# Kernel tuning notes

Measured on AMD Instinct MI355X. Metric: run time of the kernel, lower is better.

Reference implementation:

```python
import jax, jax.numpy as jnp
import numpy as np

EPS = 1e-5
OFFSET_SCALE = 1.0
KPTS = 9   # 3x3 deformable kernel
GROUP = 1  # in_dim // out_dim


def _bn(x, g, b, m, v):
    # eval-mode BatchNorm2d on (B,C,H,W)
    s = g / jnp.sqrt(v + EPS)
    return x * s[None, :, None, None] + (b - m * s)[None, :, None, None]


def _dcnv4_core(value, offset, mask, offset_scale):
    # value: (B,H,W,G,Cg); offset: (B,H,W,G,K,2) as (dx,dy); mask: (B,H,W,G,K)
    B, H, W, G, Cg = value.shape
    K = mask.shape[-1]
    dt = value.dtype
    ky = jnp.repeat(jnp.arange(3) - 1, 3).astype(dt)
    kx = jnp.tile(jnp.arange(3) - 1, 3).astype(dt)
    grid = jnp.stack([kx, ky], -1)                                   # (K,2)
    base = jnp.stack(jnp.meshgrid(jnp.arange(W, dtype=dt),
                                  jnp.arange(H, dtype=dt),
                                  indexing='xy'), -1)                # (H,W,2) = (x,y)
    loc = base[None, :, :, None, None, :] + (grid + offset) * offset_scale  # (B,H,W,G,K,2)
    px, py = loc[..., 0], loc[..., 1]
    x0 = jnp.floor(px); y0 = jnp.floor(py)
    fx = px - x0; fy = py - y0
    vflat = value.transpose(0, 3, 1, 2, 4).reshape(B, G, H * W, Cg)
    out = jnp.zeros((B, G, H * W, Cg), dt)
    corners = ((0.0, 0.0, (1 - fx) * (1 - fy)), (1.0, 0.0, fx * (1 - fy)),
               (0.0, 1.0, (1 - fx) * fy), (1.0, 1.0, fx * fy))
    for dx, dy, wgt in corners:
        xi = x0 + dx; yi = y0 + dy
        valid = ((xi >= 0) & (xi < W) & (yi >= 0) & (yi < H)).astype(dt)
        idx = (jnp.clip(yi, 0, W and H - 1) * W + jnp.clip(xi, 0, W - 1)).astype(jnp.int32)
        idx = idx.transpose(0, 3, 1, 2, 4).reshape(B, G, H * W * K)
        v = jnp.take_along_axis(vflat, idx[..., None], axis=2).reshape(B, G, H * W, K, Cg)
        w = (wgt * valid * mask).transpose(0, 3, 1, 2, 4).reshape(B, G, H * W, K)
        out = out + jnp.einsum('bgsk,bgskc->bgsc', w, v)
    return out.reshape(B, G, H, W, Cg).transpose(0, 2, 3, 1, 4).reshape(B, H, W, G * Cg)


def setup_inputs() -> dict:
    key = jax.random.key(0)
    B, C, H, W = 8, 128, 64, 64
    C_OUT = 128
    OM = ((GROUP * KPTS * 3 + 7) // 8) * 8  # 32, offset_mask padded width
    ks = jax.random.split(key, 16)
    f = jnp.float32
    sc = 1.0 / np.sqrt(C).astype(np.float32)
    return {
        'x': jax.random.normal(ks[0], (B, C, H, W), f),
        'bn1_g': jax.random.uniform(ks[1], (C,), f, 0.5, 1.5),
        'bn1_b': jax.random.normal(ks[2], (C,), f) * 0.1,
        'bn1_m': jax.random.normal(ks[3], (C,), f) * 0.1,
        'bn1_v': jax.random.uniform(ks[4], (C,), f, 0.5, 1.5),
        'w_pw0': jax.random.normal(ks[5], (C, C), f) * sc,
        'w_vp': jax.random.normal(ks[6], (C, C), f) * sc,
        'b_vp': jnp.zeros((C,), f),
        'w_om': jax.random.normal(ks[7], (C, OM), f) * 0.01,
        'b_om': jnp.zeros((OM,), f),
        'w_op': jax.random.normal(ks[8], (C, C), f) * sc,
        'bn2_g': jax.random.uniform(ks[9], (C,), f, 0.5, 1.5),
        'bn2_b': jax.random.normal(ks[10], (C,), f) * 0.1,
        'bn2_m': jax.random.normal(ks[11], (C,), f) * 0.1,
        'bn2_v': jax.random.uniform(ks[12], (C,), f, 0.5, 1.5),
        'w_pw1': jax.random.normal(ks[13], (C_OUT, C), f) * sc,
    }


def reference(x, bn1_g, bn1_b, bn1_m, bn1_v, w_pw0, w_vp, b_vp, w_om, b_om, w_op,
              bn2_g, bn2_b, bn2_m, bn2_v, w_pw1):
    x = _bn(x, bn1_g, bn1_b, bn1_m, bn1_v)
    x = jnp.einsum('bchw,oc->bohw', x, w_pw0)
    B, C, H, W = x.shape
    x = x.reshape(B, H * W, C)  # raw reshape (faithful to torch .reshape, NOT a permute)
    G, K = GROUP, KPTS
    Cg = C // G
    value = (x @ w_vp + b_vp).reshape(B, H, W, G, Cg)
    om = (x @ w_om + b_om)[..., :G * K * 3].reshape(B, H, W, G, K, 3)
    out = _dcnv4_core(value, om[..., :2], om[..., 2], OFFSET_SCALE)
    out = out.reshape(B, H * W, C) @ w_op
    x = out.reshape(B, C, H, W)  # raw reshape back
    x = _bn(x, bn2_g, bn2_b, bn2_m, bn2_v)
    x = jnp.einsum('bchw,oc->bohw', x, w_pw1)
    return x
```

## Files before the change

### kernel.cpp

```cpp
#include <hip/hip_runtime.h>

#define HW 4096
#define PADF 33
#define PADU 136
typedef unsigned short ushort;
typedef __attribute__((ext_vector_type(8))) short short8;
typedef __attribute__((ext_vector_type(4))) float f32x4;

__device__ __forceinline__ ushort bf_rne(float f) {
  unsigned u = __float_as_uint(f);
  unsigned r = (u + 0x7fffu + ((u >> 16) & 1u)) >> 16;
  return (ushort)r;
}
__device__ __forceinline__ void split2(float f, ushort& hi, ushort& lo) {
  ushort h = bf_rne(f);
  float hf = __uint_as_float((unsigned)h << 16);
  hi = h;
  lo = bf_rne(f - hf);
}

__global__ __launch_bounds__(256) void prep(
    const float* __restrict__ g1, const float* __restrict__ be1,
    const float* __restrict__ m1, const float* __restrict__ v1,
    const float* __restrict__ w0,
    const float* __restrict__ g2, const float* __restrict__ be2,
    const float* __restrict__ m2, const float* __restrict__ v2,
    const float* __restrict__ w1,
    const float* __restrict__ wvp, const float* __restrict__ wom,
    const float* __restrict__ wop,
    ushort* __restrict__ W0h, ushort* __restrict__ W0l, float* __restrict__ b0,
    ushort* __restrict__ W1h, ushort* __restrict__ W1l, float* __restrict__ b1,
    ushort* __restrict__ vph, ushort* __restrict__ vpl,
    ushort* __restrict__ oph, ushort* __restrict__ opl,
    ushort* __restrict__ omh, ushort* __restrict__ oml)
{
  const int t = threadIdx.x;
  const int role = blockIdx.x;
  if (role < 16) {
    __shared__ float sc[128], sh[128], part[16][17];
    const int cv = role >> 3;
    const float* g  = cv ? g2 : g1;
    const float* be = cv ? be2 : be1;
    const float* mm = cv ? m2 : m1;
    const float* vv = cv ? v2 : v1;
    if (t < 128) {
      float s = g[t] / sqrtf(vv[t] + 1e-5f);
      sc[t] = s;
      sh[t] = be[t] - mm[t] * s;
    }
    __syncthreads();
    const float* ws = cv ? w1 : w0;
    ushort* dh = cv ? W1h : W0h;
    ushort* dl = cv ? W1l : W0l;
    float* bb  = cv ? b1 : b0;
    const int o = ((role & 7) << 4) + (t >> 4);
    const int kl = t & 15;
    float accb = 0.f;
    #pragma unroll
    for (int j = 0; j < 8; ++j) {
      const int k = (kl << 3) + j;
      const float wv = ws[o * 128 + k];
      ushort hi, lo;
      split2(wv * sc[k], hi, lo);
      dh[o * 128 + k] = hi;
      dl[o * 128 + k] = lo;
      accb = fmaf(wv, sh[k], accb);
    }
    part[t >> 4][kl] = accb;
    __syncthreads();
    if (kl == 0) {
      float s = 0.f;
      #pragma unroll
      for (int j = 0; j < 16; ++j) s += part[t >> 4][j];
      bb[o] = s;
    }
  } else if (role < 32) {
    const int rr = role & 7;
    const float* srcM = (role < 24) ? wvp : wop;
    ushort* dh = (role < 24) ? vph : oph;
    ushort* dl = (role < 24) ? vpl : opl;
    const int n = (rr << 4) + (t >> 4);
    const int kl = t & 15;
    #pragma unroll
    for (int j = 0; j < 8; ++j) {
      const int k = (kl << 3) + j;
      ushort hi, lo;
      split2(srcM[k * 128 + n], hi, lo);
      dh[n * 128 + k] = hi;
      dl[n * 128 + k] = lo;
    }
  } else {
    const int n = ((role - 32) << 4) + (t >> 4);
    const int kl = t & 15;
    #pragma unroll
    for (int j = 0; j < 8; ++j) {
      const int k = (kl << 3) + j;
      ushort hi, lo;
      split2(wom[k * 32 + n], hi, lo);
      omh[n * 128 + k] = hi;
      oml[n * 128 + k] = lo;
    }
  }
}

__global__ __launch_bounds__(512, 2) void fused_x_valom(
    const float* __restrict__ x,
    const ushort* __restrict__ W0h, const ushort* __restrict__ W0l,
    const float* __restrict__ b0,
    const ushort* __restrict__ vph, const ushort* __restrict__ vpl,
    const float* __restrict__ bvp, const float* __restrict__ bom,
    float* __restrict__ value, float* __restrict__ omb)
{
  __shared__ __align__(16) char smem[102912];
  __shared__ float b0_s[128], b2_s[160];
  ushort (*Wh_s)[32] = (ushort(*)[32])(smem);
  ushort (*Wl_s)[32] = (ushort(*)[32])(smem + 8192);
  float*  Xf         = (float*)(smem + 16384);
  ushort (*Vh_s)[32] = (ushort(*)[32])(smem);
  ushort (*Vl_s)[32] = (ushort(*)[32])(smem + 10240);
  ushort (*Yh)[PADU] = (ushort(*)[PADU])(smem + 33280);
  ushort (*Yl)[PADU] = (ushort(*)[PADU])(smem + 68096);

  const int t = threadIdx.x;
  const int cb = blockIdx.x;
  const int b = blockIdx.y;
  const int hwBase = cb << 7;
  const size_t xbase = (size_t)b * (size_t)(128 * HW);
  if (t < 128) b0_s[t] = b0[t];
  if (t < 160) b2_s[t] = (t < 128) ? bvp[t] : bom[t - 128];
  const int lane = t & 63, w = t >> 6;
  const int col = lane & 15, quad = lane >> 4;
  const f32x4 z = {0.f, 0.f, 0.f, 0.f};

  f32x4 acc1[8];
  #pragma unroll
  for (int f = 0; f < 8; ++f) acc1[f] = z;

  for (int kc = 0; kc < 4; ++kc) {
    const int kB = kc << 5;
    {
      const int o = t >> 2, q8 = (t & 3) << 3;
      *(uint4*)&Wh_s[o][q8] = *(const uint4*)&W0h[o * 128 + kB + q8];
      *(uint4*)&Wl_s[o][q8] = *(const uint4*)&W0l[o * 128 + kB + q8];
    }
    #pragma unroll
    for (int p = 0; p < 2; ++p) {
      const int idx = (p << 9) + t;
      const int c = idx >> 5, j4 = (idx & 31) << 2;
      const float4 f = *(const float4*)&x[xbase + (size_t)(kB + c) * HW + hwBase + j4];
      Xf[(j4 + 0) * PADF + c] = f.x;
      Xf[(j4 + 1) * PADF + c] = f.y;
      Xf[(j4 + 2) * PADF + c] = f.z;
      Xf[(j4 + 3) * PADF + c] = f.w;
    }
    __syncthreads();
    union { ushort u[8]; short8 v; } bh, bl;
    {
      const float* xr = &Xf[((w << 4) + col) * PADF + (quad << 3)];
      #pragma unroll
      for (int j = 0; j < 8; ++j) split2(xr[j], bh.u[j], bl.u[j]);
    }
    #pragma unroll
    for (int f = 0; f < 8; ++f) {
      const int row = (f << 4) + col;
      const short8 aH = *(const short8*)&Wh_s[row][quad << 3];
      const short8 aL = *(const short8*)&Wl_s[row][quad << 3];
      acc1[f] = __builtin_amdgcn_mfma_f32_16x16x32_bf16(aH, bh.v, acc1[f], 0, 0, 0);
      acc1[f] = __builtin_amdgcn_mfma_f32_16x16x32_bf16(aH, bl.v, acc1[f], 0, 0, 0);
      acc1[f] = __builtin_amdgcn_mfma_f32_16x16x32_bf16(aL, bh.v, acc1[f], 0, 0, 0);
    }
    __syncthreads();
  }

  #pragma unroll
  for (int f = 0; f < 8; ++f)
    #pragma unroll
    for (int r = 0; r < 4; ++r) {
      const int o = (f << 4) + (quad << 2) + r;
      const int j = (w << 4) + col;
      ushort hi, lo;
      split2(acc1[f][r] + b0_s[o], hi, lo);
      Yh[o][j] = hi;
      Yl[o][j] = lo;
    }

  const int wm2 = (w & 3) << 5;
  const int wn2 = (w >> 2) * 80;
  f32x4 acc2[2][5];
  #pragma unroll
  for (int i = 0; i < 2; ++i)
    #pragma unroll
    for (int j = 0; j < 5; ++j) acc2[i][j] = z;

  for (int j2 = 0; j2 < 4; ++j2) {
    for (int i = t; i < 640; i += 512) {
      const int n = i >> 2, q8 = (i & 3) << 3;
      *(uint4*)&Vh_s[n][q8] = *(const uint4*)&vph[n * 128 + (j2 << 5) + q8];
      *(uint4*)&Vl_s[n][q8] = *(const uint4*)&vpl[n * 128 + (j2 << 5) + q8];
    }
    __syncthreads();
    short8 aH[2], aL[2];
    #pragma unroll
    for (int f2 = 0; f2 < 2; ++f2) {
      const int row = wm2 + (f2 << 4) + col;
      aH[f2] = *(const short8*)&Yh[row][(j2 << 5) + (quad << 3)];
      aL[f2] = *(const short8*)&Yl[row][(j2 << 5) + (quad << 3)];
    }
    #pragma unroll
    for (int g2 = 0; g2 < 5; ++g2) {
      const int n = wn2 + (g2 << 4) + col;
      const short8 vh = *(const short8*)&Vh_s[n][quad << 3];
      const short8 vl = *(const short8*)&Vl_s[n][quad << 3];
      #pragma unroll
      for (int f2 = 0; f2 < 2; ++f2) {
        acc2[f2][g2] = __builtin_amdgcn_mfma_f32_16x16x32_bf16(aH[f2], vh, acc2[f2][g2], 0, 0, 0);
        acc2[f2][g2] = __builtin_amdgcn_mfma_f32_16x16x32_bf16(aH[f2], vl, acc2[f2][g2], 0, 0, 0);
        acc2[f2][g2] = __builtin_amdgcn_mfma_f32_16x16x32_bf16(aL[f2], vh, acc2[f2][g2], 0, 0, 0);
      }
    }
    __syncthreads();
  }
  #pragma unroll
  for (int f2 = 0; f2 < 2; ++f2)
    #pragma unroll
    for (int r = 0; r < 4; ++r) {
      const int m = wm2 + (f2 << 4) + (quad << 2) + r;
      const size_t gRow = (size_t)b * HW + (size_t)m * 32 + cb;
      #pragma unroll
      for (int g2 = 0; g2 < 5; ++g2) {
        const int n = wn2 + (g2 << 4) + col;
        const float v = acc2[f2][g2][r] + b2_s[n];
        if (n < 128) value[gRow * 128 + n] = v;
        else         omb[gRow * 32 + (n - 128)] = v;
      }
    }
}

__global__ __launch_bounds__(256) void dcn_sample(
    const float* __restrict__ value, const float* __restrict__ om,
    ushort* __restrict__ samph, ushort* __restrict__ sampl)
{
  __shared__ float oms[8][32];
  const int t = threadIdx.x;
  const int blk = blockIdx.x;
  const int b = blk & 7;
  const int sBase = (blk >> 3) << 3;
  const int s = sBase + (t >> 5);
  const int cg = (t & 31) << 2;
  oms[t >> 5][t & 31] = om[((size_t)b * HW + sBase + (t >> 5)) * 32 + (t & 31)];
  __syncthreads();
  const int h = s >> 6, wq = s & 63;
  const float* vb = value + (size_t)b * HW * 128;
  const float* omp = oms[t >> 5];
  const float fw = (float)wq, fh = (float)h;
  float4 acc = {0.f, 0.f, 0.f, 0.f};
  #pragma unroll
  for (int k = 0; k < 9; ++k) {
    const float kx = (float)(k % 3 - 1);
    const float ky = (float)(k / 3 - 1);
    const float dx = omp[k * 3 + 0];
    const float dy = omp[k * 3 + 1];
    const float m  = omp[k * 3 + 2];
    const float px = fw + kx + dx;
    const float py = fh + ky + dy;
    const float x0f = floorf(px), y0f = floorf(py);
    const float fx = px - x0f, fy = py - y0f;
    const int ix = (int)x0f, iy = (int)y0f;
    #pragma unroll
    for (int cy = 0; cy < 2; ++cy) {
      const int yi = iy + cy;
      const float wy = cy ? fy : 1.f - fy;
      const float vy = (yi >= 0 && yi < 64) ? 1.f : 0.f;
      const int yc = min(max(yi, 0), 63);
      #pragma unroll
      for (int cx = 0; cx < 2; ++cx) {
        const int xi = ix + cx;
        const float wx = cx ? fx : 1.f - fx;
        const float vx = (xi >= 0 && xi < 64) ? 1.f : 0.f;
        const int xc = min(max(xi, 0), 63);
        const float wgt = wx * wy * vx * vy * m;
        const float4 v = *(const float4*)&vb[(size_t)(yc * 64 + xc) * 128 + cg];
        acc.x = fmaf(wgt, v.x, acc.x);
        acc.y = fmaf(wgt, v.y, acc.y);
        acc.z = fmaf(wgt, v.z, acc.z);
        acc.w = fmaf(wgt, v.w, acc.w);
      }
    }
  }
  ushort h0, l0, h1, l1, h2, l2, h3, l3;
  split2(acc.x, h0, l0); split2(acc.y, h1, l1);
  split2(acc.z, h2, l2); split2(acc.w, h3, l3);
  const size_t idx = ((size_t)b * HW + s) * 128 + cg;
  uint2 uh, ul;
  uh.x = (unsigned)h0 | ((unsigned)h1 << 16);
  uh.y = (unsigned)h2 | ((unsigned)h3 << 16);
  ul.x = (unsigned)l0 | ((unsigned)l1 << 16);
  ul.y = (unsigned)l2 | ((unsigned)l3 << 16);
  *(uint2*)&samph[idx] = uh;
  *(uint2*)&sampl[idx] = ul;
}

__global__ __launch_bounds__(512, 2) void fused_op_out(
    const ushort* __restrict__ samph, const ushort* __restrict__ sampl,
    const ushort* __restrict__ oph, const ushort* __restrict__ opl,
    const ushort* __restrict__ W1h, const ushort* __restrict__ W1l,
    const float* __restrict__ b1, float* __restrict__ out)
{
  __shared__ __align__(16) char smem[102400];
  __shared__ float b1_s[128];
  ushort (*Ah_s)[32]  = (ushort(*)[32])(smem);
  ushort (*Al_s)[32]  = (ushort(*)[32])(smem + 8192);
  ushort (*Bh_s)[32]  = (ushort(*)[32])(smem + 16384);
  ushort (*Bl_s)[32]  = (ushort(*)[32])(smem + 24576);
  ushort (*W1h_s)[32] = (ushort(*)[32])(smem);
  ushort (*W1l_s)[32] = (ushort(*)[32])(smem + 8192);
  ushort (*Yh)[PADU]  = (ushort(*)[PADU])(smem + 32768);
  ushort (*Yl)[PADU]  = (ushort(*)[PADU])(smem + 67584);

  const int t = threadIdx.x;
  const int cb = blockIdx.x;
  const int b = blockIdx.y;
  if (t < 128) b1_s[t] = b1[t];
  const int lane = t & 63, w = t >> 6;
  const int col = lane & 15, quad = lane >> 4;
  const f32x4 z = {0.f, 0.f, 0.f, 0.f};

  const int wm1 = (w & 1) << 6, wn1 = (w >> 1) << 5;
  f32x4 acc1[4][2];
  #pragma unroll
  for (int i = 0; i < 4; ++i) { acc1[i][0] = z; acc1[i][1] = z; }

  for (int kc = 0; kc < 4; ++kc) {
    const int kB = kc << 5;
    {
      const int m = t >> 2, q8 = (t & 3) << 3;
      const size_t row = (size_t)b * HW + (size_t)m * 32 + cb;
      *(uint4*)&Ah_s[m][q8] = *(const uint4*)&samph[row * 128 + kB + q8];
      *(uint4*)&Al_s[m][q8] = *(const uint4*)&sampl[row * 128 + kB + q8];
      *(uint4*)&Bh_s[m][q8] = *(const uint4*)&oph[m * 128 + kB + q8];
      *(uint4*)&Bl_s[m][q8] = *(const uint4*)&opl[m * 128 + kB + q8];
    }
    __syncthreads();
    short8 aH[4], aL[4];
    #pragma unroll
    for (int f = 0; f < 4; ++f) {
      const int row = wm1 + (f << 4) + col;
      aH[f] = *(const short8*)&Ah_s[row][quad << 3];
      aL[f] = *(const short8*)&Al_s[row][quad << 3];
    }
    #pragma unroll
    for (int g = 0; g < 2; ++g) {
      const int n = wn1 + (g << 4) + col;
      const short8 bh = *(const short8*)&Bh_s[n][quad << 3];
      const short8 bl = *(const short8*)&Bl_s[n][quad << 3];
      #pragma unroll
      for (int f = 0; f < 4; ++f) {
        acc1[f][g] = __builtin_amdgcn_mfma_f32_16x16x32_bf16(aH[f], bh, acc1[f][g], 0, 0, 0);
        acc1[f][g] = __builtin_amdgcn_mfma_f32_16x16x32_bf16(aH[f], bl, acc1[f][g], 0, 0, 0);
        acc1[f][g] = __builtin_amdgcn_mfma_f32_16x16x32_bf16(aL[f], bh, acc1[f][g], 0, 0, 0);
      }
    }
    __syncthreads();
  }

  #pragma unroll
  for (int f = 0; f < 4; ++f)
    #pragma unroll
    for (int g = 0; g < 2; ++g)
      #pragma unroll
      for (int r = 0; r < 4; ++r) {
        const int ch = wm1 + (f << 4) + (quad << 2) + r;
        const int j  = wn1 + (g << 4) + col;
        ushort hi, lo;
        split2(acc1[f][g][r], hi, lo);
        Yh[j][ch] = hi;
        Yl[j][ch] = lo;
      }

  const int wm2 = (w & 1) << 6, wn2 = (w >> 1) << 5;
  f32x4 acc2[4][2];
  #pragma unroll
  for (int i = 0; i < 4; ++i) { acc2[i][0] = z; acc2[i][1] = z; }

  for (int j2 = 0; j2 < 4; ++j2) {
    {
      const int o = t >> 2, q8 = (t & 3) << 3;
      *(uint4*)&W1h_s[o][q8] = *(const uint4*)&W1h[o * 128 + (j2 << 5) + q8];
      *(uint4*)&W1l_s[o][q8] = *(const uint4*)&W1l[o * 128 + (j2 << 5) + q8];
    }
    __syncthreads();
    short8 aH[4], aL[4];
    #pragma unroll
    for (int f2 = 0; f2 < 4; ++f2) {
      const int row = wm2 + (f2 << 4) + col;
      aH[f2] = *(const short8*)&W1h_s[row][quad << 3];
      aL[f2] = *(const short8*)&W1l_s[row][quad << 3];
    }
    #pragma unroll
    for (int g2 = 0; g2 < 2; ++g2) {
      const int j = wn2 + (g2 << 4) + col;
      const short8 bh = *(const short8*)&Yh[j][(j2 << 5) + (quad << 3)];
      const short8 bl = *(const short8*)&Yl[j][(j2 << 5) + (quad << 3)];
      #pragma unroll
      for (int f2 = 0; f2 < 4; ++f2) {
        acc2[f2][g2] = __builtin_amdgcn_mfma_f32_16x16x32_bf16(aH[f2], bh, acc2[f2][g2], 0, 0, 0);
        acc2[f2][g2] = __builtin_amdgcn_mfma_f32_16x16x32_bf16(aH[f2], bl, acc2[f2][g2], 0, 0, 0);
        acc2[f2][g2] = __builtin_amdgcn_mfma_f32_16x16x32_bf16(aL[f2], bh, acc2[f2][g2], 0, 0, 0);
      }
    }
    __syncthreads();
  }
  const size_t obase = (size_t)b * (size_t)(128 * HW) + ((size_t)cb << 7);
  #pragma unroll
  for (int f2 = 0; f2 < 4; ++f2)
    #pragma unroll
    for (int r = 0; r < 4; ++r) {
      const int o = wm2 + (f2 << 4) + (quad << 2) + r;
      #pragma unroll
      for (int g2 = 0; g2 < 2; ++g2) {
        const int j = wn2 + (g2 << 4) + col;
        out[obase + (size_t)o * HW + j] = acc2[f2][g2][r] + b1_s[o];
      }
    }
}

extern "C" void kernel_launch(void* const* d_in, const int* in_sizes, int n_in,
                              void* d_out, int out_size, void* d_ws, size_t ws_size,
                              hipStream_t stream)
{
  const float* x    = (const float*)d_in[0];
  const float* g1   = (const float*)d_in[1];
  const float* be1  = (const float*)d_in[2];
  const float* m1   = (const float*)d_in[3];
  const float* v1   = (const float*)d_in[4];
  const float* wpw0 = (const float*)d_in[5];
  const float* wvp  = (const float*)d_in[6];
  const float* bvp  = (const float*)d_in[7];
  const float* womW = (const float*)d_in[8];
  const float* bom  = (const float*)d_in[9];
  const float* wop  = (const float*)d_in[10];
  const float* g2   = (const float*)d_in[11];
  const float* be2  = (const float*)d_in[12];
  const float* m2   = (const float*)d_in[13];
  const float* v2   = (const float*)d_in[14];
  const float* wpw1 = (const float*)d_in[15];

  char* ws = (char*)d_ws;
  float*  value = (float*) (ws + 0);
  float*  omb   = (float*) (ws + 16777216);
  ushort* samph = (ushort*)(ws + 20971520);
  ushort* sampl = (ushort*)(ws + 29360128);
  size_t o = 37748736;
  ushort* W0h = (ushort*)(ws + o); o += 32768;
  ushort* W0l = (ushort*)(ws + o); o += 32768;
  ushort* W1h = (ushort*)(ws + o); o += 32768;
  ushort* W1l = (ushort*)(ws + o); o += 32768;
  ushort* vph = (ushort*)(ws + o); o += 40960;
  ushort* vpl = (ushort*)(ws + o); o += 40960;
  ushort* oph = (ushort*)(ws + o); o += 32768;
  ushort* opl = (ushort*)(ws + o); o += 32768;
  float*  b0  = (float*)(ws + o);  o += 512;
  float*  b1  = (float*)(ws + o);
  ushort* omh = vph + 128 * 128;
  ushort* oml = vpl + 128 * 128;

  prep<<<34, 256, 0, stream>>>(g1, be1, m1, v1, wpw0, g2, be2, m2, v2, wpw1,
                               wvp, womW, wop,
                               W0h, W0l, b0, W1h, W1l, b1,
                               vph, vpl, oph, opl, omh, oml);
  fused_x_valom<<<dim3(32, 8), 512, 0, stream>>>(x, W0h, W0l, b0, vph, vpl,
                                                 bvp, bom, value, omb);
  dcn_sample<<<dim3(4096), 256, 0, stream>>>(value, omb, samph, sampl);
  fused_op_out<<<dim3(32, 8), 512, 0, stream>>>(samph, sampl, oph, opl,
                                                W1h, W1l, b1, (float*)d_out);
}
```

Measured before the change: 148.2 us.

## Fuse deformable sampling into the op/out GEMM kernel via shared memory

Merges the dcn_sample kernel into fused_op_out. Each block now computes its 128 sampled rows straight into LDS as bf16 hi/lo pairs, and the op GEMM reads them from there. This removes the global round trip of the samph/sampl intermediates and one kernel launch. In exchange the block grid drops from 4096 small sampling blocks to 256 large blocks, so each thread holds 32 fp32 accumulators and does 9x4x8 float4 gathers, and the sampling phase has less parallelism available to hide latency.

```diff
diff --git a/kernel.cpp b/kernel.cpp
--- a/kernel.cpp
+++ b/kernel.cpp
@@ -236,25 +236,49 @@
     }
 }
 
-__global__ __launch_bounds__(256) void dcn_sample(
-    const float* __restrict__ value, const float* __restrict__ om,
-    ushort* __restrict__ samph, ushort* __restrict__ sampl)
+__global__ __launch_bounds__(512, 2) void fused_samp_op_out(
+    const float* __restrict__ value, const float* __restrict__ omb,
+    const ushort* __restrict__ oph, const ushort* __restrict__ opl,
+    const ushort* __restrict__ W1h, const ushort* __restrict__ W1l,
+    const float* __restrict__ b1, float* __restrict__ out)
 {
-  __shared__ float oms[8][32];
+  __shared__ __align__(16) char smem[86528];
+  __shared__ float b1_s[128];
+  ushort (*Ah_s)[PADU] = (ushort(*)[PADU])(smem);
+  ushort (*Al_s)[PADU] = (ushort(*)[PADU])(smem + 34816);
+  float  (*oms)[33]    = (float(*)[33])(smem + 69632);
+  ushort (*Bh_s)[32]   = (ushort(*)[32])(smem + 69632);
+  ushort (*Bl_s)[32]   = (ushort(*)[32])(smem + 77824);
+  ushort (*W1h_s)[32]  = (ushort(*)[32])(smem + 69632);
+  ushort (*W1l_s)[32]  = (ushort(*)[32])(smem + 77824);
+  ushort (*Yh)[PADU]   = (ushort(*)[PADU])(smem);
+  ushort (*Yl)[PADU]   = (ushort(*)[PADU])(smem + 34816);
+
   const int t = threadIdx.x;
   const int blk = blockIdx.x;
   const int b = blk & 7;
-  const int sBase = (blk >> 3) << 3;
-  const int s = sBase + (t >> 5);
-  const int cg = (t & 31) << 2;
-  oms[t >> 5][t & 31] = om[((size_t)b * HW + sBase + (t >> 5)) * 32 + (t & 31)];
+  const int cb = blk >> 3;
+  if (t < 128) b1_s[t] = b1[t];
+  const int lane = t & 63, w = t >> 6;
+  const int col = lane & 15, quad = lane >> 4;
+  const f32x4 z = {0.f, 0.f, 0.f, 0.f};
+
+  {
+    const int tk0 = t >> 2, jo = (t & 3) << 3;
+    const float* orow = &omb[((size_t)b * HW + (size_t)tk0 * 32 + cb) * 32 + jo];
+    *(float4*)&oms[tk0][jo]     = *(const float4*)orow;
+    *(float4*)&oms[tk0][jo + 4] = *(const float4*)(orow + 4);
+  }
   __syncthreads();
+  const int tk = t >> 2, q = t & 3;
+  const int s = tk * 32 + cb;
   const int h = s >> 6, wq = s & 63;
-  const float* vb = value + (size_t)b * HW * 128;
-  const float* omp = oms[t >> 5];
+  const float* vb = value + (size_t)b * HW * 128 + (q << 5);
+  const float* omp = oms[tk];
   const float fw = (float)wq, fh = (float)h;
-  float4 acc = {0.f, 0.f, 0.f, 0.f};
-  #pragma unroll
+  float acc[32];
+  #pragma unroll
+  for (int j = 0; j < 32; ++j) acc[j] = 0.f;
   for (int k = 0; k < 9; ++k) {
     const float kx = (float)(k % 3 - 1);
     const float ky = (float)(k / 3 - 1);
@@ -279,51 +303,26 @@
         const float vx = (xi >= 0 && xi < 64) ? 1.f : 0.f;
         const int xc = min(max(xi, 0), 63);
         const float wgt = wx * wy * vx * vy * m;
-        const float4 v = *(const float4*)&vb[(size_t)(yc * 64 + xc) * 128 + cg];
-        acc.x = fmaf(wgt, v.x, acc.x);
-        acc.y = fmaf(wgt, v.y, acc.y);
-        acc.z = fmaf(wgt, v.z, acc.z);
-        acc.w = fmaf(wgt, v.w, acc.w);
-      }
-    }
-  }
-  ushort h0, l0, h1, l1, h2, l2, h3, l3;
-  split2(acc.x, h0, l0); split2(acc.y, h1, l1);
-  split2(acc.z, h2, l2); split2(acc.w, h3, l3);
-  const size_t idx = ((size_t)b * HW + s) * 128 + cg;
-  uint2 uh, ul;
-  uh.x = (unsigned)h0 | ((unsigned)h1 << 16);
-  uh.y = (unsigned)h2 | ((unsigned)h3 << 16);
-  ul.x = (unsigned)l0 | ((unsigned)l1 << 16);
-  ul.y = (unsigned)l2 | ((unsigned)l3 << 16);
-  *(uint2*)&samph[idx] = uh;
-  *(uint2*)&sampl[idx] = ul;
-}
-
-__global__ __launch_bounds__(512, 2) void fused_op_out(
-    const ushort* __restrict__ samph, const ushort* __restrict__ sampl,
-    const ushort* __restrict__ oph, const ushort* __restrict__ opl,
-    const ushort* __restrict__ W1h, const ushort* __restrict__ W1l,
-    const float* __restrict__ b1, float* __restrict__ out)
-{
-  __shared__ __align__(16) char smem[102400];
-  __shared__ float b1_s[128];
-  ushort (*Ah_s)[32]  = (ushort(*)[32])(smem);
-  ushort (*Al_s)[32]  = (ushort(*)[32])(smem + 8192);
-  ushort (*Bh_s)[32]  = (ushort(*)[32])(smem + 16384);
-  ushort (*Bl_s)[32]  = (ushort(*)[32])(smem + 24576);
-  ushort (*W1h_s)[32] = (ushort(*)[32])(smem);
-  ushort (*W1l_s)[32] = (ushort(*)[32])(smem + 8192);
-  ushort (*Yh)[PADU]  = (ushort(*)[PADU])(smem + 32768);
-  ushort (*Yl)[PADU]  = (ushort(*)[PADU])(smem + 67584);
-
-  const int t = threadIdx.x;
-  const int cb = blockIdx.x;
-  const int b = blockIdx.y;
-  if (t < 128) b1_s[t] = b1[t];
-  const int lane = t & 63, w = t >> 6;
-  const int col = lane & 15, quad = lane >> 4;
-  const f32x4 z = {0.f, 0.f, 0.f, 0.f};
+        const float* src = vb + (size_t)(yc * 64 + xc) * 128;
+        #pragma unroll
+        for (int c4 = 0; c4 < 8; ++c4) {
+          const float4 v = *(const float4*)(src + (c4 << 2));
+          acc[c4 * 4 + 0] = fmaf(wgt, v.x, acc[c4 * 4 + 0]);
+          acc[c4 * 4 + 1] = fmaf(wgt, v.y, acc[c4 * 4 + 1]);
+          acc[c4 * 4 + 2] = fmaf(wgt, v.z, acc[c4 * 4 + 2]);
+          acc[c4 * 4 + 3] = fmaf(wgt, v.w, acc[c4 * 4 + 3]);
+        }
+      }
+    }
+  }
+  #pragma unroll
+  for (int j = 0; j < 32; ++j) {
+    ushort hi, lo;
+    split2(acc[j], hi, lo);
+    Ah_s[tk][(q << 5) + j] = hi;
+    Al_s[tk][(q << 5) + j] = lo;
+  }
+  __syncthreads();
 
   const int wm1 = (w & 1) << 6, wn1 = (w >> 1) << 5;
   f32x4 acc1[4][2];
@@ -333,20 +332,17 @@
   for (int kc = 0; kc < 4; ++kc) {
     const int kB = kc << 5;
     {
-      const int m = t >> 2, q8 = (t & 3) << 3;
-      const size_t row = (size_t)b * HW + (size_t)m * 32 + cb;
-      *(uint4*)&Ah_s[m][q8] = *(const uint4*)&samph[row * 128 + kB + q8];
-      *(uint4*)&Al_s[m][q8] = *(const uint4*)&sampl[row * 128 + kB + q8];
-      *(uint4*)&Bh_s[m][q8] = *(const uint4*)&oph[m * 128 + kB + q8];
-      *(uint4*)&Bl_s[m][q8] = *(const uint4*)&opl[m * 128 + kB + q8];
+      const int n = t >> 2, q8 = (t & 3) << 3;
+      *(uint4*)&Bh_s[n][q8] = *(const uint4*)&oph[n * 128 + kB + q8];
+      *(uint4*)&Bl_s[n][q8] = *(const uint4*)&opl[n * 128 + kB + q8];
     }
     __syncthreads();
     short8 aH[4], aL[4];
     #pragma unroll
     for (int f = 0; f < 4; ++f) {
       const int row = wm1 + (f << 4) + col;
-      aH[f] = *(const short8*)&Ah_s[row][quad << 3];
-      aL[f] = *(const short8*)&Al_s[row][quad << 3];
+      aH[f] = *(const short8*)&Ah_s[row][kB + (quad << 3)];
+      aL[f] = *(const short8*)&Al_s[row][kB + (quad << 3)];
     }
     #pragma unroll
     for (int g = 0; g < 2; ++g) {
@@ -448,9 +444,7 @@
   char* ws = (char*)d_ws;
   float*  value = (float*) (ws + 0);
   float*  omb   = (float*) (ws + 16777216);
-  ushort* samph = (ushort*)(ws + 20971520);
-  ushort* sampl = (ushort*)(ws + 29360128);
-  size_t o = 37748736;
+  size_t o = 20971520;
   ushort* W0h = (ushort*)(ws + o); o += 32768;
   ushort* W0l = (ushort*)(ws + o); o += 32768;
   ushort* W1h = (ushort*)(ws + o); o += 32768;
@@ -470,7 +464,6 @@
                                vph, vpl, oph, opl, omh, oml);
   fused_x_valom<<<dim3(32, 8), 512, 0, stream>>>(x, W0h, W0l, b0, vph, vpl,
                                                  bvp, bom, value, omb);
-  dcn_sample<<<dim3(4096), 256, 0, stream>>>(value, omb, samph, sampl);
-  fused_op_out<<<dim3(32, 8), 512, 0, stream>>>(samph, sampl, oph, opl,
-                                                W1h, W1l, b1, (float*)d_out);
-}
+  fused_samp_op_out<<<dim3(256), 512, 0, stream>>>(value, omb, oph, opl,
+                                                   W1h, W1l, b1, (float*)d_out);
+}
```

New measurement: 190.4 us. +28.4%, slower.

## Split fused GEMM kernels into two half-tiles per block to double grid size

Applied to the files above, without the earlier changes.

Both fused two-stage GEMM kernels now split their 128-wide intermediate dimension across two blocks of 256 threads, giving 512 blocks instead of 256. Each block handles 64 output channels (or 64 rows of the raw-reshape intermediate), with smaller shared-memory footprints and remapped warp tiles. This is meant to fill more CUs on the MI355X and allow more resident blocks. In exchange, the x tile (first kernel) and the sampled-input tile (second kernel) are loaded twice from global memory, once per half.

```diff
diff --git a/kernel.cpp b/kernel.cpp
--- a/kernel.cpp
+++ b/kernel.cpp
@@ -103,7 +103,7 @@
   }
 }
 
-__global__ __launch_bounds__(512, 2) void fused_x_valom(
+__global__ __launch_bounds__(256, 2) void fused_x_valom(
     const float* __restrict__ x,
     const ushort* __restrict__ W0h, const ushort* __restrict__ W0l,
     const float* __restrict__ b0,
@@ -111,41 +111,42 @@
     const float* __restrict__ bvp, const float* __restrict__ bom,
     float* __restrict__ value, float* __restrict__ omb)
 {
-  __shared__ __align__(16) char smem[102912];
-  __shared__ float b0_s[128], b2_s[160];
+  __shared__ __align__(16) char smem[55296];
+  __shared__ float b0_s[64], b2_s[160];
   ushort (*Wh_s)[32] = (ushort(*)[32])(smem);
-  ushort (*Wl_s)[32] = (ushort(*)[32])(smem + 8192);
-  float*  Xf         = (float*)(smem + 16384);
-  ushort (*Vh_s)[32] = (ushort(*)[32])(smem);
-  ushort (*Vl_s)[32] = (ushort(*)[32])(smem + 10240);
-  ushort (*Yh)[PADU] = (ushort(*)[PADU])(smem + 33280);
-  ushort (*Yl)[PADU] = (ushort(*)[PADU])(smem + 68096);
+  ushort (*Wl_s)[32] = (ushort(*)[32])(smem + 4096);
+  float*  Xf         = (float*)(smem + 8192);
+  ushort (*Yh)[PADU] = (ushort(*)[PADU])(smem);
+  ushort (*Yl)[PADU] = (ushort(*)[PADU])(smem + 17408);
+  ushort (*Vh_s)[32] = (ushort(*)[32])(smem + 34816);
+  ushort (*Vl_s)[32] = (ushort(*)[32])(smem + 45056);
 
   const int t = threadIdx.x;
   const int cb = blockIdx.x;
-  const int b = blockIdx.y;
+  const int b  = blockIdx.y;
+  const int oBase = blockIdx.z << 6;
   const int hwBase = cb << 7;
   const size_t xbase = (size_t)b * (size_t)(128 * HW);
-  if (t < 128) b0_s[t] = b0[t];
+  if (t < 64)  b0_s[t] = b0[oBase + t];
   if (t < 160) b2_s[t] = (t < 128) ? bvp[t] : bom[t - 128];
   const int lane = t & 63, w = t >> 6;
   const int col = lane & 15, quad = lane >> 4;
   const f32x4 z = {0.f, 0.f, 0.f, 0.f};
 
-  f32x4 acc1[8];
-  #pragma unroll
-  for (int f = 0; f < 8; ++f) acc1[f] = z;
+  f32x4 acc1[4][2];
+  #pragma unroll
+  for (int i = 0; i < 4; ++i) { acc1[i][0] = z; acc1[i][1] = z; }
 
   for (int kc = 0; kc < 4; ++kc) {
     const int kB = kc << 5;
     {
       const int o = t >> 2, q8 = (t & 3) << 3;
-      *(uint4*)&Wh_s[o][q8] = *(const uint4*)&W0h[o * 128 + kB + q8];
-      *(uint4*)&Wl_s[o][q8] = *(const uint4*)&W0l[o * 128 + kB + q8];
-    }
-    #pragma unroll
-    for (int p = 0; p < 2; ++p) {
-      const int idx = (p << 9) + t;
+      *(uint4*)&Wh_s[o][q8] = *(const uint4*)&W0h[(oBase + o) * 128 + kB + q8];
+      *(uint4*)&Wl_s[o][q8] = *(const uint4*)&W0l[(oBase + o) * 128 + kB + q8];
+    }
+    #pragma unroll
+    for (int p = 0; p < 4; ++p) {
+      const int idx = (p << 8) + t;
       const int c = idx >> 5, j4 = (idx & 31) << 2;
       const float4 f = *(const float4*)&x[xbase + (size_t)(kB + c) * HW + hwBase + j4];
       Xf[(j4 + 0) * PADF + c] = f.x;
@@ -154,38 +155,45 @@
       Xf[(j4 + 3) * PADF + c] = f.w;
     }
     __syncthreads();
-    union { ushort u[8]; short8 v; } bh, bl;
-    {
-      const float* xr = &Xf[((w << 4) + col) * PADF + (quad << 3)];
-      #pragma unroll
-      for (int j = 0; j < 8; ++j) split2(xr[j], bh.u[j], bl.u[j]);
-    }
-    #pragma unroll
-    for (int f = 0; f < 8; ++f) {
+    union { ushort u[8]; short8 v; } bh[2], bl[2];
+    #pragma unroll
+    for (int g = 0; g < 2; ++g) {
+      const float* xr = &Xf[((w << 5) + (g << 4) + col) * PADF + (quad << 3)];
+      #pragma unroll
+      for (int j = 0; j < 8; ++j) split2(xr[j], bh[g].u[j], bl[g].u[j]);
+    }
+    #pragma unroll
+    for (int f = 0; f < 4; ++f) {
       const int row = (f << 4) + col;
       const short8 aH = *(const short8*)&Wh_s[row][quad << 3];
       const short8 aL = *(const short8*)&Wl_s[row][quad << 3];
-      acc1[f] = __builtin_amdgcn_mfma_f32_16x16x32_bf16(aH, bh.v, acc1[f], 0, 0, 0);
-      acc1[f] = __builtin_amdgcn_mfma_f32_16x16x32_bf16(aH, bl.v, acc1[f], 0, 0, 0);
-      acc1[f] = __builtin_amdgcn_mfma_f32_16x16x32_bf16(aL, bh.v, acc1[f], 0, 0, 0);
-    }
-    __syncthreads();
-  }
-
-  #pragma unroll
-  for (int f = 0; f < 8; ++f)
+      #pragma unroll
+      for (int g = 0; g < 2; ++g) {
+        acc1[f][g] = __builtin_amdgcn_mfma_f32_16x16x32_bf16(aH, bh[g].v, acc1[f][g], 0, 0, 0);
+        acc1[f][g] = __builtin_amdgcn_mfma_f32_16x16x32_bf16(aH, bl[g].v, acc1[f][g], 0, 0, 0);
+        acc1[f][g] = __builtin_amdgcn_mfma_f32_16x16x32_bf16(aL, bh[g].v, acc1[f][g], 0, 0, 0);
+      }
+    }
+    __syncthreads();
+  }
+
+  #pragma unroll
+  for (int f = 0; f < 4; ++f)
     #pragma unroll
     for (int r = 0; r < 4; ++r) {
-      const int o = (f << 4) + (quad << 2) + r;
-      const int j = (w << 4) + col;
-      ushort hi, lo;
-      split2(acc1[f][r] + b0_s[o], hi, lo);
-      Yh[o][j] = hi;
-      Yl[o][j] = lo;
-    }
-
-  const int wm2 = (w & 3) << 5;
-  const int wn2 = (w >> 2) * 80;
+      const int m = (f << 4) + (quad << 2) + r;
+      #pragma unroll
+      for (int g = 0; g < 2; ++g) {
+        const int j = (w << 5) + (g << 4) + col;
+        ushort hi, lo;
+        split2(acc1[f][g][r] + b0_s[m], hi, lo);
+        Yh[m][j] = hi;
+        Yl[m][j] = lo;
+      }
+    }
+
+  const int wm2 = (w & 1) << 5;
+  const int wn2 = (w >> 1) * 80;
   f32x4 acc2[2][5];
   #pragma unroll
   for (int i = 0; i < 2; ++i)
@@ -193,7 +201,7 @@
     for (int j = 0; j < 5; ++j) acc2[i][j] = z;
 
   for (int j2 = 0; j2 < 4; ++j2) {
-    for (int i = t; i < 640; i += 512) {
+    for (int i = t; i < 640; i += 256) {
       const int n = i >> 2, q8 = (i & 3) << 3;
       *(uint4*)&Vh_s[n][q8] = *(const uint4*)&vph[n * 128 + (j2 << 5) + q8];
       *(uint4*)&Vl_s[n][q8] = *(const uint4*)&vpl[n * 128 + (j2 << 5) + q8];
@@ -225,7 +233,7 @@
     #pragma unroll
     for (int r = 0; r < 4; ++r) {
       const int m = wm2 + (f2 << 4) + (quad << 2) + r;
-      const size_t gRow = (size_t)b * HW + (size_t)m * 32 + cb;
+      const size_t gRow = (size_t)b * HW + (size_t)(oBase + m) * 32 + cb;
       #pragma unroll
       for (int g2 = 0; g2 < 5; ++g2) {
         const int n = wn2 + (g2 << 4) + col;
@@ -300,25 +308,26 @@
   *(uint2*)&sampl[idx] = ul;
 }
 
-__global__ __launch_bounds__(512, 2) void fused_op_out(
+__global__ __launch_bounds__(256, 2) void fused_op_out(
     const ushort* __restrict__ samph, const ushort* __restrict__ sampl,
     const ushort* __restrict__ oph, const ushort* __restrict__ opl,
     const ushort* __restrict__ W1h, const ushort* __restrict__ W1l,
     const float* __restrict__ b1, float* __restrict__ out)
 {
-  __shared__ __align__(16) char smem[102400];
+  __shared__ __align__(16) char smem[51200];
   __shared__ float b1_s[128];
   ushort (*Ah_s)[32]  = (ushort(*)[32])(smem);
   ushort (*Al_s)[32]  = (ushort(*)[32])(smem + 8192);
   ushort (*Bh_s)[32]  = (ushort(*)[32])(smem + 16384);
-  ushort (*Bl_s)[32]  = (ushort(*)[32])(smem + 24576);
-  ushort (*W1h_s)[32] = (ushort(*)[32])(smem);
-  ushort (*W1l_s)[32] = (ushort(*)[32])(smem + 8192);
-  ushort (*Yh)[PADU]  = (ushort(*)[PADU])(smem + 32768);
-  ushort (*Yl)[PADU]  = (ushort(*)[PADU])(smem + 67584);
+  ushort (*Bl_s)[32]  = (ushort(*)[32])(smem + 20480);
+  ushort (*Yh)[PADU]  = (ushort(*)[PADU])(smem);
+  ushort (*Yl)[PADU]  = (ushort(*)[PADU])(smem + 17408);
+  ushort (*W1h_s)[32] = (ushort(*)[32])(smem + 34816);
+  ushort (*W1l_s)[32] = (ushort(*)[32])(smem + 43008);
 
   const int t = threadIdx.x;
-  const int cb = blockIdx.x;
+  const int cb = blockIdx.x & 31;
+  const int jBase = (blockIdx.x >> 5) << 6;
   const int b = blockIdx.y;
   if (t < 128) b1_s[t] = b1[t];
   const int lane = t & 63, w = t >> 6;
@@ -332,13 +341,16 @@
 
   for (int kc = 0; kc < 4; ++kc) {
     const int kB = kc << 5;
-    {
-      const int m = t >> 2, q8 = (t & 3) << 3;
+    for (int i = t; i < 512; i += 256) {
+      const int m = i >> 2, q8 = (i & 3) << 3;
       const size_t row = (size_t)b * HW + (size_t)m * 32 + cb;
       *(uint4*)&Ah_s[m][q8] = *(const uint4*)&samph[row * 128 + kB + q8];
       *(uint4*)&Al_s[m][q8] = *(const uint4*)&sampl[row * 128 + kB + q8];
-      *(uint4*)&Bh_s[m][q8] = *(const uint4*)&oph[m * 128 + kB + q8];
-      *(uint4*)&Bl_s[m][q8] = *(const uint4*)&opl[m * 128 + kB + q8];
+    }
+    {
+      const int n = t >> 2, q8 = (t & 3) << 3;
+      *(uint4*)&Bh_s[n][q8] = *(const uint4*)&oph[(jBase + n) * 128 + kB + q8];
+      *(uint4*)&Bl_s[n][q8] = *(const uint4*)&opl[(jBase + n) * 128 + kB + q8];
     }
     __syncthreads();
     short8 aH[4], aL[4];
@@ -383,8 +395,8 @@
   for (int i = 0; i < 4; ++i) { acc2[i][0] = z; acc2[i][1] = z; }
 
   for (int j2 = 0; j2 < 4; ++j2) {
-    {
-      const int o = t >> 2, q8 = (t & 3) << 3;
+    for (int i = t; i < 512; i += 256) {
+      const int o = i >> 2, q8 = (i & 3) << 3;
       *(uint4*)&W1h_s[o][q8] = *(const uint4*)&W1h[o * 128 + (j2 << 5) + q8];
       *(uint4*)&W1l_s[o][q8] = *(const uint4*)&W1l[o * 128 + (j2 << 5) + q8];
     }
@@ -410,7 +422,7 @@
     }
     __syncthreads();
   }
-  const size_t obase = (size_t)b * (size_t)(128 * HW) + ((size_t)cb << 7);
+  const size_t obase = (size_t)b * (size_t)(128 * HW) + ((size_t)cb << 7) + jBase;
   #pragma unroll
   for (int f2 = 0; f2 < 4; ++f2)
     #pragma unroll
@@ -468,9 +480,9 @@
                                wvp, womW, wop,
                                W0h, W0l, b0, W1h, W1l, b1,
                                vph, vpl, oph, opl, omh, oml);
-  fused_x_valom<<<dim3(32, 8), 512, 0, stream>>>(x, W0h, W0l, b0, vph, vpl,
-                                                 bvp, bom, value, omb);
+  fused_x_valom<<<dim3(32, 8, 2), 256, 0, stream>>>(x, W0h, W0l, b0, vph, vpl,
+                                                    bvp, bom, value, omb);
   dcn_sample<<<dim3(4096), 256, 0, stream>>>(value, omb, samph, sampl);
-  fused_op_out<<<dim3(32, 8), 512, 0, stream>>>(samph, sampl, oph, opl,
+  fused_op_out<<<dim3(64, 8), 256, 0, stream>>>(samph, sampl, oph, opl,
                                                 W1h, W1l, b1, (float*)d_out);
 }
```

New measurement: 148.6 us. About the same (+0.3%).
